# Kernel tuning notes

Measured on AMD Instinct MI355X. Metric: run time of the kernel, lower is better.

Reference implementation:

```python
import jax, jax.numpy as jnp
import numpy as np

B, C_IN, C_OUT, T, K, STRIDE, PAD = 16, 256, 256, 4096, 3, 1, 1


def deform_conv1d(x, offset, weight, bias):
    # x: (B,C,T); offset: (B,2K,Tout,1) interleaved (dy,dx); weight: (O,C,K); bias: (O,)
    Bn, C, Tn = x.shape
    O, _, Kn = weight.shape
    dy = offset[:, 0::2, :, 0]  # (B,K,Tout)
    dx = offset[:, 1::2, :, 0]  # (B,K,Tout)
    Tout = dy.shape[-1]
    # offset_mode='center': subtract dcn_base_offset (y base = k-pad, x base = 0)
    base_y = jnp.arange(Kn, dtype=x.dtype) - PAD
    dy = dy - base_y[None, :, None]
    # sampling position along T: t*stride - pad + k + dy
    t0 = jnp.arange(Tout, dtype=x.dtype) * STRIDE - PAD
    py = t0[None, None, :] + jnp.arange(Kn, dtype=x.dtype)[None, :, None] + dy  # (B,K,Tout)
    i0 = jnp.floor(py)
    frac = py - i0
    i0i = i0.astype(jnp.int32)

    def gather(idx):
        valid = ((idx >= 0) & (idx < Tn)).astype(x.dtype)  # zero padding outside
        idxc = jnp.clip(idx, 0, Tn - 1).reshape(Bn, 1, Kn * Tout)
        v = jnp.take_along_axis(x, jnp.broadcast_to(idxc, (Bn, C, Kn * Tout)), axis=2)
        return v.reshape(Bn, C, Kn, Tout) * valid[:, None]

    # linear interp along T
    v = gather(i0i) * (1.0 - frac)[:, None] + gather(i0i + 1) * frac[:, None]  # (B,C,K,Tout)
    # bilinear weight along the dummy width dim (W=1, base x index 0)
    wx = jnp.maximum(0.0, 1.0 - jnp.abs(dx))  # (B,K,Tout)
    v = v * wx[:, None]
    out = jnp.einsum('bckt,ock->bot', v, weight) + bias[None, :, None]
    return out


def setup_inputs() -> dict:
    key = jax.random.key(0)
    k1, k2, k3, k4 = jax.random.split(key, 4)
    x = jax.random.normal(k1, (B, C_IN, T), dtype=jnp.float32)
    offset = jax.random.normal(k2, (B, 2 * K, T, 1), dtype=jnp.float32)
    fan_in = C_IN * K
    bound = 1.0 / np.sqrt(fan_in)
    weight = jax.random.uniform(k3, (C_OUT, C_IN, K), minval=-bound, maxval=bound, dtype=jnp.float32)
    bias = jax.random.uniform(k4, (C_OUT,), minval=-bound, maxval=bound, dtype=jnp.float32)
    return {"x": x, "offset": offset, "weight": weight, "bias": bias}


def reference(x, offset, weight, bias):
    return deform_conv1d(x, offset, weight, bias)
```

## Files before the change

### kernel.cpp

```cpp
#include <hip/hip_runtime.h>
#include <hip/hip_bf16.h>

typedef __attribute__((ext_vector_type(8))) short bf16x8;
typedef __attribute__((ext_vector_type(4))) float f32x4;

constexpr int NB = 16, CIN = 256, COUT = 256, TDIM = 4096, KS = 3, PADV = 1;
constexpr int TT = 128;
constexpr int BK = 64;
constexpr int NSTEP = 12;

typedef __attribute__((address_space(1))) const unsigned int gu32;
typedef __attribute__((address_space(3))) unsigned int lu32;

static __device__ __forceinline__ ushort f2bf(float f) {
    union { __hip_bfloat16 h; ushort u; } cv;
    cv.h = __float2bfloat16(f);
    return cv.u;
}
static __device__ __forceinline__ float bf2f(ushort u) {
    union { unsigned int u32; float f; } cv;
    cv.u32 = ((unsigned int)u) << 16;
    return cv.f;
}

__global__ __launch_bounds__(256) void prepack_w(const float* __restrict__ w,
                                                 __hip_bfloat16* __restrict__ wp) {
    int idx = blockIdx.x * 256 + threadIdx.x;
    if (idx >= NSTEP * COUT * BK) return;
    int e  = idx & 7;
    int j  = (idx >> 3) & 7;
    int o  = (idx >> 6) & (COUT - 1);
    int s  = idx >> 14;
    int k  = s % 3;
    int c  = (s / 3) * 64 + ((j ^ (o & 7)) << 3) + e;
    wp[idx] = __float2bfloat16(w[(o * CIN + c) * KS + k]);
}

__global__ __launch_bounds__(256) void transpose_x(const float* __restrict__ x,
                                                   ushort* __restrict__ xT) {
    __shared__ ushort tile[64][72];
    const int b  = blockIdx.z;
    const int c0 = blockIdx.y * 64;
    const int t0 = blockIdx.x * 64;
    const int tid = threadIdx.x;
    {
        const int c  = tid >> 2;
        const int tq = (tid & 3) << 4;
        const float* src = x + ((size_t)(b * CIN + c0 + c)) * TDIM + t0 + tq;
        #pragma unroll
        for (int i = 0; i < 4; ++i) {
            float4 f = *(const float4*)(src + 4 * i);
            tile[tq + 4 * i + 0][c] = f2bf(f.x);
            tile[tq + 4 * i + 1][c] = f2bf(f.y);
            tile[tq + 4 * i + 2][c] = f2bf(f.z);
            tile[tq + 4 * i + 3][c] = f2bf(f.w);
        }
    }
    __syncthreads();
    {
        const int t = tid >> 2;
        const int q = tid & 3;
        const uint4* lp = (const uint4*)&tile[t][q * 16];
        uint4 v0 = lp[0], v1 = lp[1];
        uint4* dst = (uint4*)(xT + ((size_t)b * TDIM + t0 + t) * CIN + c0 + q * 16);
        dst[0] = v0;
        dst[1] = v1;
    }
}

__global__ __launch_bounds__(512, 4) void deform_mfma_xt(
    const ushort* __restrict__ xT,
    const float* __restrict__ off,
    const __hip_bfloat16* __restrict__ wp,
    const float* __restrict__ bias,
    float* __restrict__ out)
{
    __shared__ ushort w_s[COUT * BK];
    __shared__ ushort v_s[TT * BK];
    __shared__ int4   sP[KS][TT];

    const int tid = threadIdx.x;

    const int bid  = blockIdx.x;
    const int q    = bid & 7;
    const int r    = bid >> 3;
    const int b    = 2 * q + (r >> 5);
    const int tt0  = (r & 31) * TT;

    if (tid < KS * TT) {
        int k = tid >> 7, j = tid & (TT - 1);
        int t = tt0 + j;
        float dyr = off[((b * 2 * KS + 2 * k) * TDIM) + t];
        float dxr = off[((b * 2 * KS + 2 * k + 1) * TDIM) + t];
        float dyk = dyr - (float)(k - PADV);
        float py  = (float)(t - PADV + k) + dyk;
        float i0f = floorf(py);
        float fr  = py - i0f;
        int i0 = (int)i0f, i1 = i0 + 1;
        float wx = fmaxf(0.0f, 1.0f - fabsf(dxr));
        float w0 = (1.0f - fr) * wx * ((i0 >= 0 && i0 < TDIM) ? 1.0f : 0.0f);
        float w1 = fr * wx * ((i1 >= 0 && i1 < TDIM) ? 1.0f : 0.0f);
        int base = min(max(i0, 0), TDIM - 2);
        bool iA = (i0 == base);
        float wa = iA ? w0 : ((i0 + 1 == base) ? w1 : 0.0f);
        float wb = iA ? w1 : ((i0 == base + 1) ? w0 : 0.0f);
        int4 p;
        p.x = base;
        p.y = __float_as_int(wa);
        p.z = __float_as_int(wb);
        p.w = 0;
        sP[k][j] = p;
    }

    const int wid    = tid >> 6;
    const int lane   = tid & 63;
    const int o_base = (wid >> 1) * 64;
    const int t_base = (wid & 1) * 64;
    const int lr     = lane & 15;
    const int lg     = lane >> 4;

    const int tg   = tid >> 3;
    const int slot = tid & 7;
    const int t0l  = tg;
    const int t1l  = tg + 64;
    const int voffA = (t0l * 128 + slot * 16) ^ ((t0l & 7) << 4);
    const int voffB = (t1l * 128 + slot * 16) ^ ((t1l & 7) << 4);

    f32x4 acc[4][4];
    #pragma unroll
    for (int i = 0; i < 4; ++i)
        #pragma unroll
        for (int j = 0; j < 4; ++j) acc[i][j] = (f32x4)0.0f;

    const ushort* xTb = xT + (size_t)b * TDIM * CIN;

    for (int cb = 0; cb < 4; ++cb) {
      const int cbase = cb * 64;
      for (int k = 0; k < 3; ++k) {
        const int s_idx = cb * 3 + k;
        __syncthreads();

        {
            const char* gbase = (const char*)wp + (size_t)s_idx * 32768 + wid * 4096 + lane * 16;
            char* lbase = (char*)w_s + wid * 4096;
            #pragma unroll
            for (int i = 0; i < 4; ++i)
                __builtin_amdgcn_global_load_lds((gu32*)(gbase + i * 1024),
                                                 (lu32*)(lbase + i * 1024), 16, 0, 0);
        }

        {
            int4 e0 = sP[k][t0l];
            int4 e1 = sP[k][t1l];
            const ushort* rowA = xTb + (size_t)e0.x * CIN + cbase + slot * 8;
            const ushort* rowB = xTb + (size_t)e1.x * CIN + cbase + slot * 8;
            bf16x8 a0 = *(const bf16x8*)rowA;
            bf16x8 a1 = *(const bf16x8*)(rowA + CIN);
            bf16x8 b0 = *(const bf16x8*)rowB;
            bf16x8 b1 = *(const bf16x8*)(rowB + CIN);
            float wa0 = __int_as_float(e0.y), wb0 = __int_as_float(e0.z);
            float wa1 = __int_as_float(e1.y), wb1 = __int_as_float(e1.z);
            bf16x8 pk0, pk1;
            #pragma unroll
            for (int i = 0; i < 8; ++i) {
                pk0[i] = (short)f2bf(bf2f((ushort)a0[i]) * wa0 + bf2f((ushort)a1[i]) * wb0);
                pk1[i] = (short)f2bf(bf2f((ushort)b0[i]) * wa1 + bf2f((ushort)b1[i]) * wb1);
            }
            *(bf16x8*)((char*)v_s + voffA) = pk0;
            *(bf16x8*)((char*)v_s + voffB) = pk1;
        }

        __syncthreads();

        #pragma unroll
        for (int kb = 0; kb < 2; ++kb) {
            const int kk = kb * 32 + lg * 8;
            bf16x8 bfr[4];
            #pragma unroll
            for (int nf = 0; nf < 4; ++nf) {
                int tc = t_base + nf * 16 + lr;
                int byte = (tc * (BK * 2) + kk * 2) ^ ((tc & 7) << 4);
                bfr[nf] = *(const bf16x8*)((const char*)v_s + byte);
            }
            #pragma unroll
            for (int mf = 0; mf < 4; ++mf) {
                int o  = o_base + mf * 16 + lr;
                int byte = (o * (BK * 2) + kk * 2) ^ ((o & 7) << 4);
                bf16x8 af = *(const bf16x8*)((const char*)w_s + byte);
                #pragma unroll
                for (int nf = 0; nf < 4; ++nf)
                    acc[mf][nf] = __builtin_amdgcn_mfma_f32_16x16x32_bf16(
                        af, bfr[nf], acc[mf][nf], 0, 0, 0);
            }
        }
      }
    }

    #pragma unroll
    for (int mf = 0; mf < 4; ++mf) {
        #pragma unroll
        for (int r2 = 0; r2 < 4; ++r2) {
            int o = o_base + mf * 16 + lg * 4 + r2;
            float bv = bias[o];
            float* orow = out + (size_t)(b * COUT + o) * TDIM + tt0 + t_base;
            #pragma unroll
            for (int nf = 0; nf < 4; ++nf)
                orow[nf * 16 + lr] = acc[mf][nf][r2] + bv;
        }
    }
}

__global__ __launch_bounds__(512, 4) void deform_mfma_gather(
    const float* __restrict__ x,
    const float* __restrict__ off,
    const __hip_bfloat16* __restrict__ wp,
    const float* __restrict__ bias,
    float* __restrict__ out)
{
    __shared__ ushort w_s[COUT * BK];
    __shared__ ushort v_s[TT * BK];
    __shared__ int4   sP[KS][TT];

    const int tid = threadIdx.x;
    const int bid  = blockIdx.x;
    const int q    = bid & 7;
    const int r    = bid >> 3;
    const int b    = 2 * q + (r >> 5);
    const int tt0  = (r & 31) * TT;

    if (tid < KS * TT) {
        int k = tid >> 7, j = tid & (TT - 1);
        int t = tt0 + j;
        float dyr = off[((b * 2 * KS + 2 * k) * TDIM) + t];
        float dxr = off[((b * 2 * KS + 2 * k + 1) * TDIM) + t];
        float py  = (float)(t - PADV + k) + dyr - (float)(k - PADV);
        float i0f = floorf(py);
        float fr  = py - i0f;
        int i0 = (int)i0f, i1 = i0 + 1;
        float wx = fmaxf(0.0f, 1.0f - fabsf(dxr));
        float w0 = (1.0f - fr) * wx * ((i0 >= 0 && i0 < TDIM) ? 1.0f : 0.0f);
        float w1 = fr * wx * ((i1 >= 0 && i1 < TDIM) ? 1.0f : 0.0f);
        int4 p;
        p.x = min(max(i0, 0), TDIM - 1);
        p.y = min(max(i1, 0), TDIM - 1);
        p.z = __float_as_int(w0);
        p.w = __float_as_int(w1);
        sP[k][j] = p;
    }

    const int wid    = tid >> 6;
    const int lane   = tid & 63;
    const int o_base = (wid >> 1) * 64;
    const int t_base = (wid & 1) * 64;
    const int lr     = lane & 15;
    const int lg     = lane >> 4;

    f32x4 acc[4][4];
    #pragma unroll
    for (int i = 0; i < 4; ++i)
        #pragma unroll
        for (int j = 0; j < 4; ++j) acc[i][j] = (f32x4)0.0f;

    const float* xb = x + (size_t)b * CIN * TDIM;

    for (int cb = 0; cb < 4; ++cb) {
      for (int k = 0; k < 3; ++k) {
        const int s_idx = cb * 3 + k;
        const int c0    = cb * 64;
        __syncthreads();
        {
            const char* gbase = (const char*)wp + (size_t)s_idx * 32768 + wid * 4096 + lane * 16;
            char* lbase = (char*)w_s + wid * 4096;
            #pragma unroll
            for (int i = 0; i < 4; ++i)
                __builtin_amdgcn_global_load_lds((gu32*)(gbase + i * 1024),
                                                 (lu32*)(lbase + i * 1024), 16, 0, 0);
        }
        {
            const int coct0 = tid >> 7;
            const int t     = tid & (TT - 1);
            int4 p = sP[k][t];
            const float* xr0 = xb + (size_t)(c0 + coct0 * 8) * TDIM;
            const float* xr1 = xr0 + (size_t)32 * TDIM;
            float g0[16], g1[16];
            #pragma unroll
            for (int i = 0; i < 8; ++i) {
                g0[2 * i]     = xr0[p.x];
                g0[2 * i + 1] = xr0[p.y];
                xr0 += TDIM;
            }
            #pragma unroll
            for (int i = 0; i < 8; ++i) {
                g1[2 * i]     = xr1[p.x];
                g1[2 * i + 1] = xr1[p.y];
                xr1 += TDIM;
            }
            float w0 = __int_as_float(p.z), w1 = __int_as_float(p.w);
            bf16x8 pk0, pk1;
            #pragma unroll
            for (int i = 0; i < 8; ++i) {
                pk0[i] = (short)f2bf(g0[2 * i] * w0 + g0[2 * i + 1] * w1);
                pk1[i] = (short)f2bf(g1[2 * i] * w0 + g1[2 * i + 1] * w1);
            }
            int row = t * (BK * 2);
            int swz = (t & 7) << 4;
            *(bf16x8*)((char*)v_s + ((row + coct0 * 16) ^ swz))       = pk0;
            *(bf16x8*)((char*)v_s + ((row + (coct0 + 4) * 16) ^ swz)) = pk1;
        }
        __syncthreads();
        #pragma unroll
        for (int kb = 0; kb < 2; ++kb) {
            const int kk = kb * 32 + lg * 8;
            bf16x8 bfr[4];
            #pragma unroll
            for (int nf = 0; nf < 4; ++nf) {
                int tc = t_base + nf * 16 + lr;
                int byte = (tc * (BK * 2) + kk * 2) ^ ((tc & 7) << 4);
                bfr[nf] = *(const bf16x8*)((const char*)v_s + byte);
            }
            #pragma unroll
            for (int mf = 0; mf < 4; ++mf) {
                int o  = o_base + mf * 16 + lr;
                int byte = (o * (BK * 2) + kk * 2) ^ ((o & 7) << 4);
                bf16x8 af = *(const bf16x8*)((const char*)w_s + byte);
                #pragma unroll
                for (int nf = 0; nf < 4; ++nf)
                    acc[mf][nf] = __builtin_amdgcn_mfma_f32_16x16x32_bf16(
                        af, bfr[nf], acc[mf][nf], 0, 0, 0);
            }
        }
      }
    }

    #pragma unroll
    for (int mf = 0; mf < 4; ++mf) {
        #pragma unroll
        for (int r2 = 0; r2 < 4; ++r2) {
            int o = o_base + mf * 16 + lg * 4 + r2;
            float bv = bias[o];
            float* orow = out + (size_t)(b * COUT + o) * TDIM + tt0 + t_base;
            #pragma unroll
            for (int nf = 0; nf < 4; ++nf)
                orow[nf * 16 + lr] = acc[mf][nf][r2] + bv;
        }
    }
}

extern "C" void kernel_launch(void* const* d_in, const int* in_sizes, int n_in,
                              void* d_out, int out_size, void* d_ws, size_t ws_size,
                              hipStream_t stream) {
    const float* x    = (const float*)d_in[0];
    const float* off  = (const float*)d_in[1];
    const float* w    = (const float*)d_in[2];
    const float* bias = (const float*)d_in[3];
    float* out = (float*)d_out;
    __hip_bfloat16* wp = (__hip_bfloat16*)d_ws;

    prepack_w<<<dim3((NSTEP * COUT * BK + 255) / 256), dim3(256), 0, stream>>>(w, wp);

    const size_t xt_off  = 512 * 1024;
    const size_t xt_need = xt_off + (size_t)NB * TDIM * CIN * sizeof(ushort);

    if (ws_size >= xt_need) {
        ushort* xT = (ushort*)((char*)d_ws + xt_off);
        transpose_x<<<dim3(TDIM / 64, CIN / 64, NB), dim3(256), 0, stream>>>(x, xT);
        deform_mfma_xt<<<dim3(512), dim3(512), 0, stream>>>(xT, off, wp, bias, out);
    } else {
        deform_mfma_gather<<<dim3(512), dim3(512), 0, stream>>>(x, off, wp, bias, out);
    }
}
```

Baseline: 71.03 us.

## Double-buffer weight and gathered-input LDS tiles to overlap loads with MFMA

Turns the per-step loop in the transposed-input kernel into a software pipeline. Weight and interpolated-input tiles now have two LDS buffers each, the next step's gather and global-to-LDS weight load are issued before the current step's MFMAs, and one barrier per step with a manual waitcnt replaces the two syncthreads. Output stores also become nontemporal. In exchange LDS use roughly doubles and launch bounds drop to 2 blocks per CU, so occupancy falls, and the hand-placed vmcnt/barrier ordering is fragile.

```diff
diff --git a/kernel.cpp b/kernel.cpp
--- a/kernel.cpp
+++ b/kernel.cpp
@@ -68,15 +68,15 @@
     }
 }
 
-__global__ __launch_bounds__(512, 4) void deform_mfma_xt(
+__global__ __launch_bounds__(512, 2) void deform_mfma_xt(
     const ushort* __restrict__ xT,
     const float* __restrict__ off,
     const __hip_bfloat16* __restrict__ wp,
     const float* __restrict__ bias,
     float* __restrict__ out)
 {
-    __shared__ ushort w_s[COUT * BK];
-    __shared__ ushort v_s[TT * BK];
+    __shared__ ushort w_s[2][COUT * BK];
+    __shared__ ushort v_s[2][TT * BK];
     __shared__ int4   sP[KS][TT];
 
     const int tid = threadIdx.x;
@@ -109,7 +109,7 @@
         p.y = __float_as_int(wa);
         p.z = __float_as_int(wb);
         p.w = 0;
-        sP[k][j] = p;
+        sP[k][tid & (TT - 1)] = p;
     }
 
     const int wid    = tid >> 6;
@@ -134,66 +134,95 @@
 
     const ushort* xTb = xT + (size_t)b * TDIM * CIN;
 
-    for (int cb = 0; cb < 4; ++cb) {
-      const int cbase = cb * 64;
-      for (int k = 0; k < 3; ++k) {
-        const int s_idx = cb * 3 + k;
-        __syncthreads();
-
-        {
-            const char* gbase = (const char*)wp + (size_t)s_idx * 32768 + wid * 4096 + lane * 16;
-            char* lbase = (char*)w_s + wid * 4096;
-            #pragma unroll
-            for (int i = 0; i < 4; ++i)
-                __builtin_amdgcn_global_load_lds((gu32*)(gbase + i * 1024),
-                                                 (lu32*)(lbase + i * 1024), 16, 0, 0);
-        }
-
-        {
-            int4 e0 = sP[k][t0l];
-            int4 e1 = sP[k][t1l];
-            const ushort* rowA = xTb + (size_t)e0.x * CIN + cbase + slot * 8;
-            const ushort* rowB = xTb + (size_t)e1.x * CIN + cbase + slot * 8;
-            bf16x8 a0 = *(const bf16x8*)rowA;
-            bf16x8 a1 = *(const bf16x8*)(rowA + CIN);
-            bf16x8 b0 = *(const bf16x8*)rowB;
-            bf16x8 b1 = *(const bf16x8*)(rowB + CIN);
-            float wa0 = __int_as_float(e0.y), wb0 = __int_as_float(e0.z);
-            float wa1 = __int_as_float(e1.y), wb1 = __int_as_float(e1.z);
-            bf16x8 pk0, pk1;
-            #pragma unroll
-            for (int i = 0; i < 8; ++i) {
-                pk0[i] = (short)f2bf(bf2f((ushort)a0[i]) * wa0 + bf2f((ushort)a1[i]) * wb0);
-                pk1[i] = (short)f2bf(bf2f((ushort)b0[i]) * wa1 + bf2f((ushort)b1[i]) * wb1);
-            }
-            *(bf16x8*)((char*)v_s + voffA) = pk0;
-            *(bf16x8*)((char*)v_s + voffB) = pk1;
-        }
-
-        __syncthreads();
-
-        #pragma unroll
-        for (int kb = 0; kb < 2; ++kb) {
-            const int kk = kb * 32 + lg * 8;
-            bf16x8 bfr[4];
-            #pragma unroll
-            for (int nf = 0; nf < 4; ++nf) {
-                int tc = t_base + nf * 16 + lr;
-                int byte = (tc * (BK * 2) + kk * 2) ^ ((tc & 7) << 4);
-                bfr[nf] = *(const bf16x8*)((const char*)v_s + byte);
-            }
-            #pragma unroll
-            for (int mf = 0; mf < 4; ++mf) {
-                int o  = o_base + mf * 16 + lr;
-                int byte = (o * (BK * 2) + kk * 2) ^ ((o & 7) << 4);
-                bf16x8 af = *(const bf16x8*)((const char*)w_s + byte);
-                #pragma unroll
-                for (int nf = 0; nf < 4; ++nf)
-                    acc[mf][nf] = __builtin_amdgcn_mfma_f32_16x16x32_bf16(
-                        af, bfr[nf], acc[mf][nf], 0, 0, 0);
-            }
-        }
-      }
+#define STAGE_W(SIDX, BUF) do {                                                     \
+    const char* gb_ = (const char*)wp + (size_t)(SIDX) * 32768 + wid * 4096 + lane * 16; \
+    char* lb_ = (char*)w_s[BUF] + wid * 4096;                                       \
+    __builtin_amdgcn_global_load_lds((gu32*)(gb_),        (lu32*)(lb_),        16, 0, 0); \
+    __builtin_amdgcn_global_load_lds((gu32*)(gb_ + 1024), (lu32*)(lb_ + 1024), 16, 0, 0); \
+    __builtin_amdgcn_global_load_lds((gu32*)(gb_ + 2048), (lu32*)(lb_ + 2048), 16, 0, 0); \
+    __builtin_amdgcn_global_load_lds((gu32*)(gb_ + 3072), (lu32*)(lb_ + 3072), 16, 0, 0); \
+} while (0)
+
+#define GATHER(SN) do {                                                             \
+    int kn_  = (SN) % 3;                                                            \
+    int cbn_ = ((SN) / 3) * 64;                                                     \
+    int4 e0_ = sP[kn_][t0l];                                                        \
+    int4 e1_ = sP[kn_][t1l];                                                        \
+    const ushort* rA_ = xTb + (size_t)e0_.x * CIN + cbn_ + slot * 8;                \
+    const ushort* rB_ = xTb + (size_t)e1_.x * CIN + cbn_ + slot * 8;                \
+    ga0 = *(const bf16x8*)rA_;                                                      \
+    ga1 = *(const bf16x8*)(rA_ + CIN);                                              \
+    gb0 = *(const bf16x8*)rB_;                                                      \
+    gb1 = *(const bf16x8*)(rB_ + CIN);                                              \
+    wa0 = __int_as_float(e0_.y); wb0 = __int_as_float(e0_.z);                       \
+    wa1 = __int_as_float(e1_.y); wb1 = __int_as_float(e1_.z);                       \
+} while (0)
+
+#define INTERP() do {                                                               \
+    _Pragma("unroll")                                                               \
+    for (int i_ = 0; i_ < 8; ++i_) {                                                \
+        pk0[i_] = (short)f2bf(bf2f((ushort)ga0[i_]) * wa0 + bf2f((ushort)ga1[i_]) * wb0); \
+        pk1[i_] = (short)f2bf(bf2f((ushort)gb0[i_]) * wa1 + bf2f((ushort)gb1[i_]) * wb1); \
+    }                                                                               \
+} while (0)
+
+#define MFMA_PHASE(P) do {                                                          \
+    _Pragma("unroll")                                                               \
+    for (int kb = 0; kb < 2; ++kb) {                                                \
+        const int kk = kb * 32 + lg * 8;                                            \
+        bf16x8 bfr[4];                                                              \
+        _Pragma("unroll")                                                           \
+        for (int nf = 0; nf < 4; ++nf) {                                            \
+            int tc = t_base + nf * 16 + lr;                                         \
+            int byte = (tc * 128 + kk * 2) ^ ((tc & 7) << 4);                       \
+            bfr[nf] = *(const bf16x8*)((const char*)v_s[P] + byte);                 \
+        }                                                                           \
+        _Pragma("unroll")                                                           \
+        for (int mf = 0; mf < 4; ++mf) {                                            \
+            int o = o_base + mf * 16 + lr;                                          \
+            int byte = (o * 128 + kk * 2) ^ ((o & 7) << 4);                         \
+            bf16x8 af = *(const bf16x8*)((const char*)w_s[P] + byte);               \
+            _Pragma("unroll")                                                       \
+            for (int nf = 0; nf < 4; ++nf)                                          \
+                acc[mf][nf] = __builtin_amdgcn_mfma_f32_16x16x32_bf16(              \
+                    af, bfr[nf], acc[mf][nf], 0, 0, 0);                             \
+        }                                                                           \
+    }                                                                               \
+} while (0)
+
+    __syncthreads();
+
+    bf16x8 ga0, ga1, gb0, gb1, pk0, pk1;
+    float wa0, wb0, wa1, wb1;
+    STAGE_W(0, 0);
+    GATHER(0);
+    INTERP();
+
+    #pragma unroll 1
+    for (int s = 0; s < NSTEP - 1; ++s) {
+        const int p = s & 1;
+        *(bf16x8*)((char*)v_s[p] + voffA) = pk0;
+        *(bf16x8*)((char*)v_s[p] + voffB) = pk1;
+        GATHER(s + 1);
+        __builtin_amdgcn_sched_barrier(0);
+        asm volatile("s_waitcnt vmcnt(4) lgkmcnt(0)" ::: "memory");
+        __builtin_amdgcn_sched_barrier(0);
+        __builtin_amdgcn_s_barrier();
+        __builtin_amdgcn_sched_barrier(0);
+        STAGE_W(s + 1, p ^ 1);
+        MFMA_PHASE(p);
+        INTERP();
+    }
+
+    {
+        *(bf16x8*)((char*)v_s[1] + voffA) = pk0;
+        *(bf16x8*)((char*)v_s[1] + voffB) = pk1;
+        __builtin_amdgcn_sched_barrier(0);
+        asm volatile("s_waitcnt vmcnt(0) lgkmcnt(0)" ::: "memory");
+        __builtin_amdgcn_sched_barrier(0);
+        __builtin_amdgcn_s_barrier();
+        __builtin_amdgcn_sched_barrier(0);
+        MFMA_PHASE(1);
     }
 
     #pragma unroll
@@ -205,9 +234,13 @@
             float* orow = out + (size_t)(b * COUT + o) * TDIM + tt0 + t_base;
             #pragma unroll
             for (int nf = 0; nf < 4; ++nf)
-                orow[nf * 16 + lr] = acc[mf][nf][r2] + bv;
-        }
-    }
+                __builtin_nontemporal_store(acc[mf][nf][r2] + bv, &orow[nf * 16 + lr]);
+        }
+    }
+#undef STAGE_W
+#undef GATHER
+#undef INTERP
+#undef MFMA_PHASE
 }
 
 __global__ __launch_bounds__(512, 4) void deform_mfma_gather(
```

Result: slower. 78.25 us (+10.2%).

## Load weight MFMA fragments directly from global and shrink tiles to more blocks

Applied to the files above, without the earlier changes.

The main kernel no longer stages the weight tile in LDS. A new prepack kernel lays the bf16 weights out in MFMA fragment order, so each lane loads its A operands straight from global memory (L2-resident). The block tile shrinks to 64 time steps by 128 output channels with 256 threads, which gives 2048 blocks and less LDS per block for higher occupancy. In exchange, the deformed-sample gather for each time tile is now repeated for both output-channel halves, and weight traffic from global grows.

```diff
diff --git a/kernel.cpp b/kernel.cpp
--- a/kernel.cpp
+++ b/kernel.cpp
@@ -5,8 +5,7 @@
 typedef __attribute__((ext_vector_type(4))) float f32x4;
 
 constexpr int NB = 16, CIN = 256, COUT = 256, TDIM = 4096, KS = 3, PADV = 1;
-constexpr int TT = 128;
-constexpr int BK = 64;
+constexpr int TT = 64;
 constexpr int NSTEP = 12;
 
 typedef __attribute__((address_space(1))) const unsigned int gu32;
@@ -23,10 +22,27 @@
     return cv.f;
 }
 
+__global__ __launch_bounds__(256) void prepack_w2(const float* __restrict__ w,
+                                                  __hip_bfloat16* __restrict__ wp2) {
+    int idx = blockIdx.x * 256 + threadIdx.x;
+    if (idx >= NSTEP * COUT * 64) return;
+    int e    = idx & 7;
+    int lane = (idx >> 3) & 63;
+    int mf   = (idx >> 9) & 1;
+    int kb   = (idx >> 10) & 1;
+    int wid  = (idx >> 11) & 3;
+    int ot   = (idx >> 13) & 1;
+    int s    = idx >> 14;
+    int o = ot * 128 + wid * 32 + mf * 16 + (lane & 15);
+    int k = s % 3;
+    int c = (s / 3) * 64 + kb * 32 + (lane >> 4) * 8 + e;
+    wp2[idx] = __float2bfloat16(w[(o * CIN + c) * KS + k]);
+}
+
 __global__ __launch_bounds__(256) void prepack_w(const float* __restrict__ w,
                                                  __hip_bfloat16* __restrict__ wp) {
     int idx = blockIdx.x * 256 + threadIdx.x;
-    if (idx >= NSTEP * COUT * BK) return;
+    if (idx >= NSTEP * COUT * 64) return;
     int e  = idx & 7;
     int j  = (idx >> 3) & 7;
     int o  = (idx >> 6) & (COUT - 1);
@@ -68,27 +84,28 @@
     }
 }
 
-__global__ __launch_bounds__(512, 4) void deform_mfma_xt(
+__global__ __launch_bounds__(256, 4) void deform_mfma_xt(
     const ushort* __restrict__ xT,
     const float* __restrict__ off,
-    const __hip_bfloat16* __restrict__ wp,
+    const ushort* __restrict__ wp2,
     const float* __restrict__ bias,
     float* __restrict__ out)
 {
-    __shared__ ushort w_s[COUT * BK];
-    __shared__ ushort v_s[TT * BK];
+    __shared__ ushort v_s[TT * 64];
     __shared__ int4   sP[KS][TT];
 
     const int tid = threadIdx.x;
 
-    const int bid  = blockIdx.x;
-    const int q    = bid & 7;
-    const int r    = bid >> 3;
-    const int b    = 2 * q + (r >> 5);
-    const int tt0  = (r & 31) * TT;
+    const int bid = blockIdx.x;
+    const int q   = bid & 7;
+    const int r   = bid >> 3;
+    const int b   = 2 * q + (r >> 7);
+    const int r2  = r & 127;
+    const int ot  = r2 >> 6;
+    const int tt0 = (r2 & 63) * TT;
 
     if (tid < KS * TT) {
-        int k = tid >> 7, j = tid & (TT - 1);
+        int k = tid >> 6, j = tid & (TT - 1);
         int t = tt0 + j;
         float dyr = off[((b * 2 * KS + 2 * k) * TDIM) + t];
         float dxr = off[((b * 2 * KS + 2 * k + 1) * TDIM) + t];
@@ -112,23 +129,21 @@
         sP[k][j] = p;
     }
 
-    const int wid    = tid >> 6;
-    const int lane   = tid & 63;
-    const int o_base = (wid >> 1) * 64;
-    const int t_base = (wid & 1) * 64;
-    const int lr     = lane & 15;
-    const int lg     = lane >> 4;
+    const int wid  = tid >> 6;
+    const int lane = tid & 63;
+    const int lr   = lane & 15;
+    const int lg   = lane >> 4;
 
     const int tg   = tid >> 3;
     const int slot = tid & 7;
     const int t0l  = tg;
-    const int t1l  = tg + 64;
+    const int t1l  = tg + 32;
     const int voffA = (t0l * 128 + slot * 16) ^ ((t0l & 7) << 4);
     const int voffB = (t1l * 128 + slot * 16) ^ ((t1l & 7) << 4);
 
-    f32x4 acc[4][4];
+    f32x4 acc[2][4];
     #pragma unroll
-    for (int i = 0; i < 4; ++i)
+    for (int i = 0; i < 2; ++i)
         #pragma unroll
         for (int j = 0; j < 4; ++j) acc[i][j] = (f32x4)0.0f;
 
@@ -140,14 +155,12 @@
         const int s_idx = cb * 3 + k;
         __syncthreads();
 
-        {
-            const char* gbase = (const char*)wp + (size_t)s_idx * 32768 + wid * 4096 + lane * 16;
-            char* lbase = (char*)w_s + wid * 4096;
-            #pragma unroll
-            for (int i = 0; i < 4; ++i)
-                __builtin_amdgcn_global_load_lds((gu32*)(gbase + i * 1024),
-                                                 (lu32*)(lbase + i * 1024), 16, 0, 0);
-        }
+        const ushort* wslot = wp2 + (size_t)(((s_idx * 2 + ot) * 4 + wid) * 4) * 512
+                                  + lane * 8;
+        bf16x8 af00 = *(const bf16x8*)(wslot);
+        bf16x8 af01 = *(const bf16x8*)(wslot + 512);
+        bf16x8 af10 = *(const bf16x8*)(wslot + 1024);
+        bf16x8 af11 = *(const bf16x8*)(wslot + 1536);
 
         {
             int4 e0 = sP[k][t0l];
@@ -178,34 +191,31 @@
             bf16x8 bfr[4];
             #pragma unroll
             for (int nf = 0; nf < 4; ++nf) {
-                int tc = t_base + nf * 16 + lr;
-                int byte = (tc * (BK * 2) + kk * 2) ^ ((tc & 7) << 4);
+                int tc = nf * 16 + lr;
+                int byte = (tc * 128 + kk * 2) ^ ((tc & 7) << 4);
                 bfr[nf] = *(const bf16x8*)((const char*)v_s + byte);
             }
-            #pragma unroll
-            for (int mf = 0; mf < 4; ++mf) {
-                int o  = o_base + mf * 16 + lr;
-                int byte = (o * (BK * 2) + kk * 2) ^ ((o & 7) << 4);
-                bf16x8 af = *(const bf16x8*)((const char*)w_s + byte);
-                #pragma unroll
-                for (int nf = 0; nf < 4; ++nf)
-                    acc[mf][nf] = __builtin_amdgcn_mfma_f32_16x16x32_bf16(
-                        af, bfr[nf], acc[mf][nf], 0, 0, 0);
+            bf16x8 a0 = kb ? af10 : af00;
+            bf16x8 a1 = kb ? af11 : af01;
+            #pragma unroll
+            for (int nf = 0; nf < 4; ++nf) {
+                acc[0][nf] = __builtin_amdgcn_mfma_f32_16x16x32_bf16(a0, bfr[nf], acc[0][nf], 0, 0, 0);
+                acc[1][nf] = __builtin_amdgcn_mfma_f32_16x16x32_bf16(a1, bfr[nf], acc[1][nf], 0, 0, 0);
             }
         }
       }
     }
 
     #pragma unroll
-    for (int mf = 0; mf < 4; ++mf) {
-        #pragma unroll
-        for (int r2 = 0; r2 < 4; ++r2) {
-            int o = o_base + mf * 16 + lg * 4 + r2;
+    for (int mf = 0; mf < 2; ++mf) {
+        #pragma unroll
+        for (int rg = 0; rg < 4; ++rg) {
+            int o = ot * 128 + wid * 32 + mf * 16 + lg * 4 + rg;
             float bv = bias[o];
-            float* orow = out + (size_t)(b * COUT + o) * TDIM + tt0 + t_base;
+            float* orow = out + (size_t)(b * COUT + o) * TDIM + tt0;
             #pragma unroll
             for (int nf = 0; nf < 4; ++nf)
-                orow[nf * 16 + lr] = acc[mf][nf][r2] + bv;
+                orow[nf * 16 + lr] = acc[mf][nf][rg] + bv;
         }
     }
 }
@@ -217,19 +227,19 @@
     const float* __restrict__ bias,
     float* __restrict__ out)
 {
-    __shared__ ushort w_s[COUT * BK];
-    __shared__ ushort v_s[TT * BK];
-    __shared__ int4   sP[KS][TT];
+    __shared__ ushort w_s[COUT * 64];
+    __shared__ ushort v_s[128 * 64];
+    __shared__ int4   sP[KS][128];
 
     const int tid = threadIdx.x;
     const int bid  = blockIdx.x;
     const int q    = bid & 7;
     const int r    = bid >> 3;
     const int b    = 2 * q + (r >> 5);
-    const int tt0  = (r & 31) * TT;
-
-    if (tid < KS * TT) {
-        int k = tid >> 7, j = tid & (TT - 1);
+    const int tt0  = (r & 31) * 128;
+
+    if (tid < KS * 128) {
+        int k = tid >> 7, j = tid & 127;
         int t = tt0 + j;
         float dyr = off[((b * 2 * KS + 2 * k) * TDIM) + t];
         float dxr = off[((b * 2 * KS + 2 * k + 1) * TDIM) + t];
@@ -278,7 +288,7 @@
         }
         {
             const int coct0 = tid >> 7;
-            const int t     = tid & (TT - 1);
+            const int t     = tid & 127;
             int4 p = sP[k][t];
             const float* xr0 = xb + (size_t)(c0 + coct0 * 8) * TDIM;
             const float* xr1 = xr0 + (size_t)32 * TDIM;
@@ -302,7 +312,7 @@
                 pk0[i] = (short)f2bf(g0[2 * i] * w0 + g0[2 * i + 1] * w1);
                 pk1[i] = (short)f2bf(g1[2 * i] * w0 + g1[2 * i + 1] * w1);
             }
-            int row = t * (BK * 2);
+            int row = t * 128;
             int swz = (t & 7) << 4;
             *(bf16x8*)((char*)v_s + ((row + coct0 * 16) ^ swz))       = pk0;
             *(bf16x8*)((char*)v_s + ((row + (coct0 + 4) * 16) ^ swz)) = pk1;
@@ -315,13 +325,13 @@
             #pragma unroll
             for (int nf = 0; nf < 4; ++nf) {
                 int tc = t_base + nf * 16 + lr;
-                int byte = (tc * (BK * 2) + kk * 2) ^ ((tc & 7) << 4);
+                int byte = (tc * 128 + kk * 2) ^ ((tc & 7) << 4);
                 bfr[nf] = *(const bf16x8*)((const char*)v_s + byte);
             }
             #pragma unroll
             for (int mf = 0; mf < 4; ++mf) {
                 int o  = o_base + mf * 16 + lr;
-                int byte = (o * (BK * 2) + kk * 2) ^ ((o & 7) << 4);
+                int byte = (o * 128 + kk * 2) ^ ((o & 7) << 4);
                 bf16x8 af = *(const bf16x8*)((const char*)w_s + byte);
                 #pragma unroll
                 for (int nf = 0; nf < 4; ++nf)
@@ -335,13 +345,13 @@
     #pragma unroll
     for (int mf = 0; mf < 4; ++mf) {
         #pragma unroll
-        for (int r2 = 0; r2 < 4; ++r2) {
-            int o = o_base + mf * 16 + lg * 4 + r2;
+        for (int rg = 0; rg < 4; ++rg) {
+            int o = o_base + mf * 16 + lg * 4 + rg;
             float bv = bias[o];
             float* orow = out + (size_t)(b * COUT + o) * TDIM + tt0 + t_base;
             #pragma unroll
             for (int nf = 0; nf < 4; ++nf)
-                orow[nf * 16 + lr] = acc[mf][nf][r2] + bv;
+                orow[nf * 16 + lr] = acc[mf][nf][rg] + bv;
         }
     }
 }
@@ -354,18 +364,19 @@
     const float* w    = (const float*)d_in[2];
     const float* bias = (const float*)d_in[3];
     float* out = (float*)d_out;
-    __hip_bfloat16* wp = (__hip_bfloat16*)d_ws;
-
-    prepack_w<<<dim3((NSTEP * COUT * BK + 255) / 256), dim3(256), 0, stream>>>(w, wp);
 
     const size_t xt_off  = 512 * 1024;
     const size_t xt_need = xt_off + (size_t)NB * TDIM * CIN * sizeof(ushort);
 
     if (ws_size >= xt_need) {
-        ushort* xT = (ushort*)((char*)d_ws + xt_off);
+        ushort* wp2 = (ushort*)d_ws;
+        ushort* xT  = (ushort*)((char*)d_ws + xt_off);
+        prepack_w2<<<dim3(768), dim3(256), 0, stream>>>(w, (__hip_bfloat16*)wp2);
         transpose_x<<<dim3(TDIM / 64, CIN / 64, NB), dim3(256), 0, stream>>>(x, xT);
-        deform_mfma_xt<<<dim3(512), dim3(512), 0, stream>>>(xT, off, wp, bias, out);
+        deform_mfma_xt<<<dim3(2048), dim3(256), 0, stream>>>(xT, off, wp2, bias, out);
     } else {
+        __hip_bfloat16* wp = (__hip_bfloat16*)d_ws;
+        prepack_w<<<dim3(768), dim3(256), 0, stream>>>(w, wp);
         deform_mfma_gather<<<dim3(512), dim3(512), 0, stream>>>(x, off, wp, bias, out);
     }
 }
```

After: 68.79 us. -3.1%, faster.
